# Kernel tuning notes

Measured on AMD Instinct MI355X. Metric: run time of the kernel, lower is better.

## Reference

```python
import jax, jax.numpy as jnp
import numpy as np

EPS = 1e-5
SLOPE = 0.2

def _inorm(x):
    # InstanceNorm2d with affine=False on [B, C, N, 1]: normalize over spatial N per (b, c).
    mu = jnp.mean(x, axis=-1, keepdims=True)
    var = jnp.var(x, axis=-1, keepdims=True)  # biased variance, matches torch InstanceNorm
    return (x - mu) * jax.lax.rsqrt(var + EPS)

def _lrelu(x):
    return jnp.where(x >= 0, x, SLOPE * x)

def _block(W, x):
    # 1x1 conv (channel matmul) -> instance norm -> leaky relu; x: [B, Cin, N]
    return _lrelu(_inorm(jnp.einsum('oc,bcn->bon', W, x)))

def setup_inputs() -> dict:
    key = jax.random.key(0)
    k1, k2, k3, k4, k5 = jax.random.split(key, 5)
    B, C, N = 8, 256, 2048
    feat = jax.random.normal(k1, (B, C, N), dtype=jnp.float32)
    W1 = jax.random.normal(k2, (2 * C, C), dtype=jnp.float32) * (1.0 / np.sqrt(C))
    W2 = jax.random.normal(k3, (2 * C, C), dtype=jnp.float32) * (1.0 / np.sqrt(C))
    W3 = jax.random.normal(k4, (2 * C, C), dtype=jnp.float32) * (1.0 / np.sqrt(C))
    W4 = jax.random.normal(k5, (C, 2 * C), dtype=jnp.float32) * (1.0 / np.sqrt(2 * C))
    return {"feat": feat, "W1": W1, "W2": W2, "W3": W3, "W4": W4}

def reference(feat, W1, W2, W3, W4):
    # feat: [B, C, N]
    x1 = _block(W1, feat)  # [B, 2C, N]
    x2 = _block(W2, feat)  # [B, 2C, N]
    x3 = _block(W3, feat)  # [B, 2C, N]
    # query_key: x1^T @ x2 -> [B, N, N]
    qk = jnp.einsum('bcn,bcm->bnm', x1, x2)
    # x3 @ qk -> [B, 2C, N]; offset attention: subtract from x1
    x4 = x1 - jnp.einsum('bcn,bnm->bcm', x3, qk)
    out = _block(W4, x4)  # [B, C, N]
    return out
```

## Files before the change

### kernel.cpp

```cpp
#include <hip/hip_runtime.h>
#include <stdint.h>


#define LRELU_SLOPE 0.2f
#define EPS_IN 1e-5f

typedef __attribute__((ext_vector_type(8))) short short8v;
typedef __attribute__((ext_vector_type(4))) float f32x4;

__device__ __forceinline__ unsigned short f2bf(float f) {
    unsigned int u = __builtin_bit_cast(unsigned int, f);
    u = (u + 0x7fffu + ((u >> 16) & 1u)) >> 16;
    return (unsigned short)u;
}
__device__ __forceinline__ float bf2f(unsigned short h) {
    return __builtin_bit_cast(float, (unsigned int)h << 16);
}

typedef const __attribute__((address_space(1))) unsigned int* as1_uint_ptr;
typedef __attribute__((address_space(3))) unsigned int* as3_uint_ptr;

#define GLL16(g, l) __builtin_amdgcn_global_load_lds( \
    (as1_uint_ptr)(const void*)(g), (as3_uint_ptr)(void*)(l), 16, 0, 0)

enum { EP_F32 = 0, EP_BF16 = 1, EP_SUB_T_SPLIT = 2, EP_BF16_STATS = 3 };

template<int BM, int BN, int EP>
__global__ __launch_bounds__(256)
void gemm_tn(const unsigned short* __restrict__ A, const unsigned short* __restrict__ B,
             const unsigned short* __restrict__ Dm, void* __restrict__ Cv,
             float2* __restrict__ part,
             int K, int lda, int ldb, int ldd, int ldc,
             int64_t sA, int64_t sB, int64_t sD, int64_t sC)
{
    constexpr int FM = BM / 32, FN = BN / 32;
    const int bz = blockIdx.z;
    A += sA * bz;
    B += sB * bz;

    const int i0 = blockIdx.y * BM;
    const int j0 = blockIdx.x * BN;

    __shared__ __align__(16) unsigned short As[2][BM * 32];
    __shared__ __align__(16) unsigned short Bs[2][BN * 32];

    const int t = threadIdx.x;
    const int w = t >> 6, l = t & 63;
    const int wr = w >> 1, wc = w & 1;
    const int srow = l >> 2, skq = (l & 3) * 8;

    f32x4 acc[FM][FN];
#pragma unroll
    for (int fm = 0; fm < FM; ++fm)
#pragma unroll
        for (int fn = 0; fn < FN; ++fn)
            acc[fm][fn] = (f32x4){0.f, 0.f, 0.f, 0.f};

    const int NT = K / 32;

#pragma unroll
    for (int q = 0; q < BM / 64; ++q) {
        const int seg = w * (BM / 64) + q;
        GLL16(A + (size_t)(i0 + seg * 16 + srow) * lda + skq, &As[0][seg * 512]);
    }
#pragma unroll
    for (int q = 0; q < BN / 64; ++q) {
        const int seg = w * (BN / 64) + q;
        GLL16(B + (size_t)(j0 + seg * 16 + srow) * ldb + skq, &Bs[0][seg * 512]);
    }
    __syncthreads();

    for (int tt = 0; tt < NT; ++tt) {
        const int cur = tt & 1;
        if (tt + 1 < NT) {
            const int k0 = (tt + 1) * 32;
#pragma unroll
            for (int q = 0; q < BM / 64; ++q) {
                const int seg = w * (BM / 64) + q;
                GLL16(A + (size_t)(i0 + seg * 16 + srow) * lda + k0 + skq, &As[cur ^ 1][seg * 512]);
            }
#pragma unroll
            for (int q = 0; q < BN / 64; ++q) {
                const int seg = w * (BN / 64) + q;
                GLL16(B + (size_t)(j0 + seg * 16 + srow) * ldb + k0 + skq, &Bs[cur ^ 1][seg * 512]);
            }
        }
        short8v a[FM], b[FN];
#pragma unroll
        for (int fm = 0; fm < FM; ++fm)
            a[fm] = *(const short8v*)&As[cur][(wr * (BM / 2) + fm * 16 + (l & 15)) * 32 + (l >> 4) * 8];
#pragma unroll
        for (int fn = 0; fn < FN; ++fn)
            b[fn] = *(const short8v*)&Bs[cur][(wc * (BN / 2) + fn * 16 + (l & 15)) * 32 + (l >> 4) * 8];
#pragma unroll
        for (int fm = 0; fm < FM; ++fm)
#pragma unroll
            for (int fn = 0; fn < FN; ++fn)
                acc[fm][fn] = __builtin_amdgcn_mfma_f32_16x16x32_bf16(a[fm], b[fn], acc[fm][fn], 0, 0, 0);
        __syncthreads();
    }

    const int cr4 = (l >> 4) * 4;
    const int cc = l & 15;

    if constexpr (EP == EP_F32) {
        float* C = (float*)Cv + sC * bz;
#pragma unroll
        for (int fm = 0; fm < FM; ++fm)
#pragma unroll
            for (int fn = 0; fn < FN; ++fn)
#pragma unroll
                for (int r = 0; r < 4; ++r)
                    C[(size_t)(i0 + wr * (BM / 2) + fm * 16 + cr4 + r) * ldc +
                      (j0 + wc * (BN / 2) + fn * 16 + cc)] = acc[fm][fn][r];
    } else if constexpr (EP == EP_BF16) {
        unsigned short* C = (unsigned short*)Cv + sC * bz;
#pragma unroll
        for (int fm = 0; fm < FM; ++fm)
#pragma unroll
            for (int fn = 0; fn < FN; ++fn)
#pragma unroll
                for (int r = 0; r < 4; ++r)
                    C[(size_t)(i0 + wr * (BM / 2) + fm * 16 + cr4 + r) * ldc +
                      (j0 + wc * (BN / 2) + fn * 16 + cc)] = f2bf(acc[fm][fn][r]);
    } else if constexpr (EP == EP_SUB_T_SPLIT) {
        const unsigned short* D = Dm + sD * bz;
        unsigned short* C = (unsigned short*)Cv + sC * bz;
#pragma unroll
        for (int fm = 0; fm < FM; ++fm) {
            const int grow0 = i0 + wr * (BM / 2) + fm * 16 + cr4;
#pragma unroll
            for (int fn = 0; fn < FN; ++fn) {
                const int gcol = j0 + wc * (BN / 2) + fn * 16 + cc;
                ushort4 hi4, lo4;
#pragma unroll
                for (int r = 0; r < 4; ++r) {
                    const float sv = bf2f(D[(size_t)(grow0 + r) * ldd + gcol]) - acc[fm][fn][r];
                    const unsigned short h = f2bf(sv);
                    ((unsigned short*)&hi4)[r] = h;
                    ((unsigned short*)&lo4)[r] = f2bf(sv - bf2f(h));
                }
                *(ushort4*)&C[(size_t)gcol * ldc + grow0] = hi4;
                *(ushort4*)&C[(size_t)gcol * ldc + (ldc >> 1) + grow0] = lo4;
            }
        }
    } else {
        unsigned short* C = (unsigned short*)Cv + sC * bz;
        __shared__ float2 wp[2][BM];
#pragma unroll
        for (int fm = 0; fm < FM; ++fm) {
#pragma unroll
            for (int r = 0; r < 4; ++r) {
                float s = 0.f, q = 0.f;
#pragma unroll
                for (int fn = 0; fn < FN; ++fn) {
                    const float v = acc[fm][fn][r];
                    s += v; q += v * v;
                    C[(size_t)(i0 + wr * (BM / 2) + fm * 16 + cr4 + r) * ldc +
                      (j0 + wc * (BN / 2) + fn * 16 + cc)] = f2bf(v);
                }
#pragma unroll
                for (int m = 1; m < 16; m <<= 1) {
                    s += __shfl_xor(s, m, 64);
                    q += __shfl_xor(q, m, 64);
                }
                if ((l & 15) == 0)
                    wp[wc][wr * (BM / 2) + fm * 16 + cr4 + r] = make_float2(s, q);
            }
        }
        __syncthreads();
        if (t < BM) {
            const float2 p0 = wp[0][t], p1 = wp[1][t];
            part[(size_t)(bz * 1536 + i0 + t) * gridDim.x + blockIdx.x] =
                make_float2(p0.x + p1.x, p0.y + p1.y);
        }
    }
}

__global__ __launch_bounds__(256)
void reduce_stats(const float2* __restrict__ part, float2* __restrict__ stats)
{
    const int row = blockIdx.x * 256 + threadIdx.x;
    float S = 0.f, Q = 0.f;
#pragma unroll
    for (int j = 0; j < 16; ++j) {
        const float2 p = part[(size_t)row * 16 + j];
        S += p.x; Q += p.y;
    }
    const float mu = S * (1.0f / 2048.0f);
    const float var = Q * (1.0f / 2048.0f) - mu * mu;
    stats[row] = make_float2(mu, rsqrtf(var + EPS_IN));
}

__device__ __forceinline__ uint4 norm8(uint4 v, float2 st)
{
    const unsigned int wd[4] = {v.x, v.y, v.z, v.w};
    unsigned int o[4];
#pragma unroll
    for (int i = 0; i < 4; ++i) {
        float a = __builtin_bit_cast(float, wd[i] << 16);
        float b = __builtin_bit_cast(float, wd[i] & 0xffff0000u);
        a = (a - st.x) * st.y; a = a >= 0.f ? a : LRELU_SLOPE * a;
        b = (b - st.x) * st.y; b = b >= 0.f ? b : LRELU_SLOPE * b;
        o[i] = (unsigned int)f2bf(a) | ((unsigned int)f2bf(b) << 16);
    }
    return make_uint4(o[0], o[1], o[2], o[3]);
}

__global__ __launch_bounds__(256)
void normx(const unsigned short* __restrict__ ybf, const float2* __restrict__ stats,
           unsigned short* __restrict__ x2T, unsigned short* __restrict__ x1n3)
{
    const int b = blockIdx.x;
    const int t = threadIdx.x;
    if (b < 2048) {
        __shared__ __align__(16) unsigned short tile[64][68];
        const int bx = b & 31, by = (b >> 5) & 7, bz = b >> 8;
        const unsigned short* in = ybf + (size_t)bz * 3145728 + (size_t)512 * 2048;
        unsigned short* outp = x2T + (size_t)bz * 1048576;
        const int r0 = by * 64, c0 = bx * 64;
        const int ir = t >> 4, ic = (t & 15) * 4;
#pragma unroll
        for (int q = 0; q < 4; ++q) {
            const int rr = q * 16 + ir;
            const float2 st = stats[bz * 1536 + 512 + r0 + rr];
            const ushort4 v = *(const ushort4*)&in[(size_t)(r0 + rr) * 2048 + c0 + ic];
            const unsigned short vv[4] = {v.x, v.y, v.z, v.w};
#pragma unroll
            for (int j = 0; j < 4; ++j) {
                float e = (bf2f(vv[j]) - st.x) * st.y;
                e = e >= 0.f ? e : LRELU_SLOPE * e;
                tile[rr][ic + j] = f2bf(e);
            }
        }
        __syncthreads();
        const int n = t & 63, kc = (t >> 6) * 16;
        unsigned short* op = outp + (size_t)(c0 + n) * 512 + r0 + kc;
        unsigned int wo[8];
#pragma unroll
        for (int i = 0; i < 8; ++i)
            wo[i] = (unsigned int)tile[kc + 2 * i][n] | ((unsigned int)tile[kc + 2 * i + 1][n] << 16);
        *(uint4*)op       = make_uint4(wo[0], wo[1], wo[2], wo[3]);
        *(uint4*)(op + 8) = make_uint4(wo[4], wo[5], wo[6], wo[7]);
    } else {
        const int r = b - 2048;
        const int x = r & 1023, bz = r >> 10;
        const int src = (x < 512) ? x : (x + 512);
        const float2 st = stats[bz * 1536 + src];
        const uint4 v = ((const uint4*)(ybf + (size_t)bz * 3145728 + (size_t)src * 2048))[t];
        ((uint4*)(x1n3 + (size_t)bz * 2097152 + (size_t)x * 2048))[t] = norm8(v, st);
    }
}

__global__ __launch_bounds__(256)
void prep(const float* __restrict__ W1, const float* __restrict__ W2,
          const float* __restrict__ W3, const float* __restrict__ W4,
          unsigned short* __restrict__ Wcatb, unsigned short* __restrict__ W4cat,
          const float* __restrict__ feat, unsigned short* __restrict__ featT)
{
    const int b = blockIdx.x;
    const int t = threadIdx.x;
    if (b < 512) {
        const int wsel = b >> 7;
        const int local = ((b & 127) * 256 + t) * 4;
        const float* src = (wsel == 0) ? W1 : (wsel == 1) ? W2 : (wsel == 2) ? W3 : W4;
        const float4 v = *(const float4*)(src + local);
        const ushort4 pk = make_ushort4(f2bf(v.x), f2bf(v.y), f2bf(v.z), f2bf(v.w));
        if (wsel < 3) {
            *(ushort4*)(Wcatb + (size_t)wsel * 131072 + local) = pk;
        } else {
            const int o = local >> 9, c = local & 511;
            *(ushort4*)(W4cat + (size_t)o * 1024 + c)       = pk;
            *(ushort4*)(W4cat + (size_t)o * 1024 + 512 + c) = pk;
        }
    } else {
        __shared__ __align__(16) unsigned short tile[64][68];
        const int r = b - 512;
        const int bx = r & 31, by = (r >> 5) & 3, bz = r >> 7;
        const float* ip0 = feat + (size_t)bz * 524288;
        unsigned short* outp = featT + (size_t)bz * 524288;
        const int r0 = by * 64, c0 = bx * 64;
        const int ir = t >> 4, ic = (t & 15) * 4;
#pragma unroll
        for (int q = 0; q < 4; ++q) {
            const int rr = q * 16 + ir;
            const float4 v = *(const float4*)&ip0[(size_t)(r0 + rr) * 2048 + c0 + ic];
            tile[rr][ic + 0] = f2bf(v.x);
            tile[rr][ic + 1] = f2bf(v.y);
            tile[rr][ic + 2] = f2bf(v.z);
            tile[rr][ic + 3] = f2bf(v.w);
        }
        __syncthreads();
        const int n = t & 63, kc = (t >> 6) * 16;
        unsigned short* op = outp + (size_t)(c0 + n) * 256 + r0 + kc;
        unsigned int wo[8];
#pragma unroll
        for (int i = 0; i < 8; ++i)
            wo[i] = (unsigned int)tile[kc + 2 * i][n] | ((unsigned int)tile[kc + 2 * i + 1][n] << 16);
        *(uint4*)op       = make_uint4(wo[0], wo[1], wo[2], wo[3]);
        *(uint4*)(op + 8) = make_uint4(wo[4], wo[5], wo[6], wo[7]);
    }
}

__global__ __launch_bounds__(256)
void row_norm_lrelu(const float* __restrict__ in, float* __restrict__ out)
{
    const size_t row = blockIdx.x;
    const float4* p = (const float4*)(in + row * 2048);
    float4* q = (float4*)(out + row * 2048);
    const int t = threadIdx.x;

    float4 v0 = p[t];
    float4 v1 = p[t + 256];

    float s  = v0.x + v0.y + v0.z + v0.w + v1.x + v1.y + v1.z + v1.w;
    float ss = v0.x * v0.x + v0.y * v0.y + v0.z * v0.z + v0.w * v0.w +
               v1.x * v1.x + v1.y * v1.y + v1.z * v1.z + v1.w * v1.w;
#pragma unroll
    for (int off = 32; off > 0; off >>= 1) {
        s  += __shfl_down(s, off, 64);
        ss += __shfl_down(ss, off, 64);
    }
    __shared__ float red[10];
    const int wid = t >> 6;
    if ((t & 63) == 0) { red[wid] = s; red[4 + wid] = ss; }
    __syncthreads();
    if (t == 0) {
        const float S  = red[0] + red[1] + red[2] + red[3];
        const float SS = red[4] + red[5] + red[6] + red[7];
        const float mu = S * (1.0f / 2048.0f);
        const float var = SS * (1.0f / 2048.0f) - mu * mu;
        red[8] = mu;
        red[9] = rsqrtf(var + EPS_IN);
    }
    __syncthreads();
    const float mu = red[8], rs = red[9];
#define NRM(x) { float e = ((x) - mu) * rs; (x) = (e >= 0.0f) ? e : LRELU_SLOPE * e; }
    NRM(v0.x) NRM(v0.y) NRM(v0.z) NRM(v0.w)
    NRM(v1.x) NRM(v1.y) NRM(v1.z) NRM(v1.w)
#undef NRM
    q[t] = v0;
    q[t + 256] = v1;
}

extern "C" void kernel_launch(void* const* d_in, const int* in_sizes, int n_in,
                              void* d_out, int out_size, void* d_ws, size_t ws_size,
                              hipStream_t stream)
{
    const float* feat = (const float*)d_in[0];
    const float* W1   = (const float*)d_in[1];
    const float* W2   = (const float*)d_in[2];
    const float* W3   = (const float*)d_in[3];
    const float* W4   = (const float*)d_in[4];
    float* out = (float*)d_out;

    char* w = (char*)d_ws;
    unsigned short* ybf   = (unsigned short*)(w + 0);
    unsigned short* x4Ts  = (unsigned short*)(w + 0);
    float*          z     = (float*)(w + 33554432);
    unsigned short* featT = (unsigned short*)(w + 50331648);
    unsigned short* x2T   = (unsigned short*)(w + 58720256);
    unsigned short* x1n3  = (unsigned short*)(w + 75497472);
    unsigned short* Amb   = (unsigned short*)(w + 109051904);
    unsigned short* Wcatb = (unsigned short*)(w + 113246208);
    unsigned short* W4cat = (unsigned short*)(w + 114032640);
    float2*         part1 = (float2*)(w + 114556928);
    float2*         stats = (float2*)(w + 116129792);

    prep<<<1536, 256, 0, stream>>>(W1, W2, W3, W4, Wcatb, W4cat, feat, featT);

    gemm_tn<128, 128, EP_BF16_STATS><<<dim3(16, 12, 8), 256, 0, stream>>>(
        Wcatb, featT, nullptr, ybf, part1,
        256, 256, 256, 0, 2048, 0, 524288, 0, 3145728);

    reduce_stats<<<48, 256, 0, stream>>>(part1, stats);

    normx<<<10240, 256, 0, stream>>>(ybf, stats, x2T, x1n3);

    gemm_tn<64, 64, EP_BF16><<<dim3(8, 8, 8), 256, 0, stream>>>(
        x1n3 + 1048576 , x1n3 , nullptr, Amb, nullptr,
        2048, 2048, 2048, 0, 512, 2097152, 2097152, 0, 262144);

    gemm_tn<128, 128, EP_SUB_T_SPLIT><<<dim3(16, 4, 8), 256, 0, stream>>>(
        Amb, x2T, x1n3, x4Ts, nullptr,
        512, 512, 512, 2048, 1024, 262144, 1048576, 2097152, 2097152);

    gemm_tn<128, 64, EP_F32><<<dim3(32, 2, 8), 256, 0, stream>>>(
        W4cat, x4Ts, nullptr, z, nullptr,
        1024, 1024, 1024, 0, 2048, 0, 2097152, 0, 524288);

    row_norm_lrelu<<<2048, 256, 0, stream>>>(z, out);
}
```

Measured before the change: 210.4 us.

## Fuse x1/x3 normalization into Gram GEMM and subtract epilogue, drop x1n3 buffer

```diff
diff --git a/kernel.cpp b/kernel.cpp
--- a/kernel.cpp
+++ b/kernel.cpp
@@ -23,13 +23,28 @@
 #define GLL16(g, l) __builtin_amdgcn_global_load_lds( \
     (as1_uint_ptr)(const void*)(g), (as3_uint_ptr)(void*)(l), 16, 0, 0)
 
-enum { EP_F32 = 0, EP_BF16 = 1, EP_SUB_T_SPLIT = 2, EP_BF16_STATS = 3 };
+enum { EP_F32 = 0, EP_BF16_STATS = 1, EP_SUB_T_SPLIT_NORM = 2 };
+
+__device__ __forceinline__ uint4 norm8(uint4 v, float2 st)
+{
+    const unsigned int wd[4] = {v.x, v.y, v.z, v.w};
+    unsigned int o[4];
+#pragma unroll
+    for (int i = 0; i < 4; ++i) {
+        float a = __builtin_bit_cast(float, wd[i] << 16);
+        float b = __builtin_bit_cast(float, wd[i] & 0xffff0000u);
+        a = (a - st.x) * st.y; a = a >= 0.f ? a : LRELU_SLOPE * a;
+        b = (b - st.x) * st.y; b = b >= 0.f ? b : LRELU_SLOPE * b;
+        o[i] = (unsigned int)f2bf(a) | ((unsigned int)f2bf(b) << 16);
+    }
+    return make_uint4(o[0], o[1], o[2], o[3]);
+}
 
 template<int BM, int BN, int EP>
 __global__ __launch_bounds__(256)
 void gemm_tn(const unsigned short* __restrict__ A, const unsigned short* __restrict__ B,
              const unsigned short* __restrict__ Dm, void* __restrict__ Cv,
-             float2* __restrict__ part,
+             const float2* __restrict__ stats, float2* __restrict__ part,
              int K, int lda, int ldb, int ldd, int ldc,
              int64_t sA, int64_t sB, int64_t sD, int64_t sC)
 {
@@ -113,29 +128,24 @@
                 for (int r = 0; r < 4; ++r)
                     C[(size_t)(i0 + wr * (BM / 2) + fm * 16 + cr4 + r) * ldc +
                       (j0 + wc * (BN / 2) + fn * 16 + cc)] = acc[fm][fn][r];
-    } else if constexpr (EP == EP_BF16) {
-        unsigned short* C = (unsigned short*)Cv + sC * bz;
-#pragma unroll
-        for (int fm = 0; fm < FM; ++fm)
-#pragma unroll
-            for (int fn = 0; fn < FN; ++fn)
-#pragma unroll
-                for (int r = 0; r < 4; ++r)
-                    C[(size_t)(i0 + wr * (BM / 2) + fm * 16 + cr4 + r) * ldc +
-                      (j0 + wc * (BN / 2) + fn * 16 + cc)] = f2bf(acc[fm][fn][r]);
-    } else if constexpr (EP == EP_SUB_T_SPLIT) {
+    } else if constexpr (EP == EP_SUB_T_SPLIT_NORM) {
         const unsigned short* D = Dm + sD * bz;
         unsigned short* C = (unsigned short*)Cv + sC * bz;
 #pragma unroll
         for (int fm = 0; fm < FM; ++fm) {
             const int grow0 = i0 + wr * (BM / 2) + fm * 16 + cr4;
+            float2 st[4];
+#pragma unroll
+            for (int r = 0; r < 4; ++r) st[r] = stats[bz * 1536 + grow0 + r];
 #pragma unroll
             for (int fn = 0; fn < FN; ++fn) {
                 const int gcol = j0 + wc * (BN / 2) + fn * 16 + cc;
                 ushort4 hi4, lo4;
 #pragma unroll
                 for (int r = 0; r < 4; ++r) {
-                    const float sv = bf2f(D[(size_t)(grow0 + r) * ldd + gcol]) - acc[fm][fn][r];
+                    float dv = (bf2f(D[(size_t)(grow0 + r) * ldd + gcol]) - st[r].x) * st[r].y;
+                    dv = dv >= 0.f ? dv : LRELU_SLOPE * dv;
+                    const float sv = dv - acc[fm][fn][r];
                     const unsigned short h = f2bf(sv);
                     ((unsigned short*)&hi4)[r] = h;
                     ((unsigned short*)&lo4)[r] = f2bf(sv - bf2f(h));
@@ -178,6 +188,74 @@
 }
 
 __global__ __launch_bounds__(256)
+void gemm_am(const unsigned short* __restrict__ ybf, const float2* __restrict__ stats,
+             unsigned short* __restrict__ Amb)
+{
+    const int bz = blockIdx.z;
+    const unsigned short* Yb = ybf + (size_t)bz * 3145728;
+    const int i0 = blockIdx.y * 64;
+    const int j0 = blockIdx.x * 64;
+
+    __shared__ __align__(16) unsigned short As[64 * 32];
+    __shared__ __align__(16) unsigned short Bs[64 * 32];
+
+    const int t = threadIdx.x, w = t >> 6, l = t & 63;
+    const int wr = w >> 1, wc = w & 1;
+    const int srow = t >> 2;
+    const int skq = (t & 3) * 8;
+
+    const float2 stA = stats[bz * 1536 + 1024 + i0 + srow];
+    const float2 stB = stats[bz * 1536 + j0 + srow];
+    const unsigned short* gA = Yb + (size_t)(1024 + i0 + srow) * 2048 + skq;
+    const unsigned short* gB = Yb + (size_t)(j0 + srow) * 2048 + skq;
+
+    f32x4 acc[2][2];
+#pragma unroll
+    for (int fm = 0; fm < 2; ++fm)
+#pragma unroll
+        for (int fn = 0; fn < 2; ++fn)
+            acc[fm][fn] = (f32x4){0.f, 0.f, 0.f, 0.f};
+
+    uint4 vA = *(const uint4*)gA;
+    uint4 vB = *(const uint4*)gB;
+
+    for (int tt = 0; tt < 64; ++tt) {
+        if (tt) __syncthreads();
+        *(uint4*)&As[srow * 32 + skq] = norm8(vA, stA);
+        *(uint4*)&Bs[srow * 32 + skq] = norm8(vB, stB);
+        if (tt + 1 < 64) {
+            vA = *(const uint4*)(gA + (size_t)(tt + 1) * 32);
+            vB = *(const uint4*)(gB + (size_t)(tt + 1) * 32);
+        }
+        __syncthreads();
+
+        short8v a[2], b[2];
+#pragma unroll
+        for (int fm = 0; fm < 2; ++fm)
+            a[fm] = *(const short8v*)&As[(wr * 32 + fm * 16 + (l & 15)) * 32 + (l >> 4) * 8];
+#pragma unroll
+        for (int fn = 0; fn < 2; ++fn)
+            b[fn] = *(const short8v*)&Bs[(wc * 32 + fn * 16 + (l & 15)) * 32 + (l >> 4) * 8];
+#pragma unroll
+        for (int fm = 0; fm < 2; ++fm)
+#pragma unroll
+            for (int fn = 0; fn < 2; ++fn)
+                acc[fm][fn] = __builtin_amdgcn_mfma_f32_16x16x32_bf16(a[fm], b[fn], acc[fm][fn], 0, 0, 0);
+    }
+
+    unsigned short* C = Amb + (size_t)bz * 262144;
+    const int cr4 = (l >> 4) * 4, cc = l & 15;
+#pragma unroll
+    for (int fm = 0; fm < 2; ++fm)
+#pragma unroll
+        for (int fn = 0; fn < 2; ++fn)
+#pragma unroll
+            for (int r = 0; r < 4; ++r)
+                C[(size_t)(i0 + wr * 32 + fm * 16 + cr4 + r) * 512 +
+                  (j0 + wc * 32 + fn * 16 + cc)] = f2bf(acc[fm][fn][r]);
+}
+
+__global__ __launch_bounds__(256)
 void reduce_stats(const float2* __restrict__ part, float2* __restrict__ stats)
 {
     const int row = blockIdx.x * 256 + threadIdx.x;
@@ -192,64 +270,41 @@
     stats[row] = make_float2(mu, rsqrtf(var + EPS_IN));
 }
 
-__device__ __forceinline__ uint4 norm8(uint4 v, float2 st)
-{
-    const unsigned int wd[4] = {v.x, v.y, v.z, v.w};
-    unsigned int o[4];
-#pragma unroll
-    for (int i = 0; i < 4; ++i) {
-        float a = __builtin_bit_cast(float, wd[i] << 16);
-        float b = __builtin_bit_cast(float, wd[i] & 0xffff0000u);
-        a = (a - st.x) * st.y; a = a >= 0.f ? a : LRELU_SLOPE * a;
-        b = (b - st.x) * st.y; b = b >= 0.f ? b : LRELU_SLOPE * b;
-        o[i] = (unsigned int)f2bf(a) | ((unsigned int)f2bf(b) << 16);
-    }
-    return make_uint4(o[0], o[1], o[2], o[3]);
-}
-
-__global__ __launch_bounds__(256)
-void normx(const unsigned short* __restrict__ ybf, const float2* __restrict__ stats,
-           unsigned short* __restrict__ x2T, unsigned short* __restrict__ x1n3)
-{
-    const int b = blockIdx.x;
-    const int t = threadIdx.x;
-    if (b < 2048) {
-        __shared__ __align__(16) unsigned short tile[64][68];
-        const int bx = b & 31, by = (b >> 5) & 7, bz = b >> 8;
-        const unsigned short* in = ybf + (size_t)bz * 3145728 + (size_t)512 * 2048;
-        unsigned short* outp = x2T + (size_t)bz * 1048576;
-        const int r0 = by * 64, c0 = bx * 64;
-        const int ir = t >> 4, ic = (t & 15) * 4;
-#pragma unroll
-        for (int q = 0; q < 4; ++q) {
-            const int rr = q * 16 + ir;
-            const float2 st = stats[bz * 1536 + 512 + r0 + rr];
-            const ushort4 v = *(const ushort4*)&in[(size_t)(r0 + rr) * 2048 + c0 + ic];
-            const unsigned short vv[4] = {v.x, v.y, v.z, v.w};
-#pragma unroll
-            for (int j = 0; j < 4; ++j) {
-                float e = (bf2f(vv[j]) - st.x) * st.y;
-                e = e >= 0.f ? e : LRELU_SLOPE * e;
-                tile[rr][ic + j] = f2bf(e);
-            }
-        }
-        __syncthreads();
-        const int n = t & 63, kc = (t >> 6) * 16;
-        unsigned short* op = outp + (size_t)(c0 + n) * 512 + r0 + kc;
-        unsigned int wo[8];
-#pragma unroll
-        for (int i = 0; i < 8; ++i)
-            wo[i] = (unsigned int)tile[kc + 2 * i][n] | ((unsigned int)tile[kc + 2 * i + 1][n] << 16);
-        *(uint4*)op       = make_uint4(wo[0], wo[1], wo[2], wo[3]);
-        *(uint4*)(op + 8) = make_uint4(wo[4], wo[5], wo[6], wo[7]);
-    } else {
-        const int r = b - 2048;
-        const int x = r & 1023, bz = r >> 10;
-        const int src = (x < 512) ? x : (x + 512);
-        const float2 st = stats[bz * 1536 + src];
-        const uint4 v = ((const uint4*)(ybf + (size_t)bz * 3145728 + (size_t)src * 2048))[t];
-        ((uint4*)(x1n3 + (size_t)bz * 2097152 + (size_t)x * 2048))[t] = norm8(v, st);
-    }
+__global__ __launch_bounds__(256)
+void transpose_norm_x2(const unsigned short* __restrict__ ybf,
+                       const float2* __restrict__ stats,
+                       unsigned short* __restrict__ x2T)
+{
+    __shared__ __align__(16) unsigned short tile[64][68];
+    const int t = threadIdx.x, bz = blockIdx.z;
+    const unsigned short* in = ybf + (size_t)bz * 3145728 + (size_t)512 * 2048;
+    unsigned short* outp = x2T + (size_t)bz * 1048576;
+    const int r0 = blockIdx.y * 64, c0 = blockIdx.x * 64;
+    const int ir = t >> 4, ic = (t & 15) * 4;
+
+#pragma unroll
+    for (int q = 0; q < 4; ++q) {
+        const int rr = q * 16 + ir;
+        const float2 st = stats[bz * 1536 + 512 + r0 + rr];
+        const ushort4 v = *(const ushort4*)&in[(size_t)(r0 + rr) * 2048 + c0 + ic];
+        const unsigned short vv[4] = {v.x, v.y, v.z, v.w};
+#pragma unroll
+        for (int j = 0; j < 4; ++j) {
+            float e = (bf2f(vv[j]) - st.x) * st.y;
+            e = e >= 0.f ? e : LRELU_SLOPE * e;
+            tile[rr][ic + j] = f2bf(e);
+        }
+    }
+    __syncthreads();
+
+    const int n = t & 63, kc = (t >> 6) * 16;
+    unsigned short* op = outp + (size_t)(c0 + n) * 512 + r0 + kc;
+    unsigned int wo[8];
+#pragma unroll
+    for (int i = 0; i < 8; ++i)
+        wo[i] = (unsigned int)tile[kc + 2 * i][n] | ((unsigned int)tile[kc + 2 * i + 1][n] << 16);
+    *(uint4*)op       = make_uint4(wo[0], wo[1], wo[2], wo[3]);
+    *(uint4*)(op + 8) = make_uint4(wo[4], wo[5], wo[6], wo[7]);
 }
 
 __global__ __launch_bounds__(256)
@@ -356,37 +411,34 @@
 
     char* w = (char*)d_ws;
     unsigned short* ybf   = (unsigned short*)(w + 0);
-    unsigned short* x4Ts  = (unsigned short*)(w + 0);
-    float*          z     = (float*)(w + 33554432);
     unsigned short* featT = (unsigned short*)(w + 50331648);
     unsigned short* x2T   = (unsigned short*)(w + 58720256);
-    unsigned short* x1n3  = (unsigned short*)(w + 75497472);
+    unsigned short* x4Ts  = (unsigned short*)(w + 75497472);
     unsigned short* Amb   = (unsigned short*)(w + 109051904);
     unsigned short* Wcatb = (unsigned short*)(w + 113246208);
     unsigned short* W4cat = (unsigned short*)(w + 114032640);
     float2*         part1 = (float2*)(w + 114556928);
     float2*         stats = (float2*)(w + 116129792);
+    float*          z     = (float*)(w + 116228096);
 
     prep<<<1536, 256, 0, stream>>>(W1, W2, W3, W4, Wcatb, W4cat, feat, featT);
 
     gemm_tn<128, 128, EP_BF16_STATS><<<dim3(16, 12, 8), 256, 0, stream>>>(
-        Wcatb, featT, nullptr, ybf, part1,
+        Wcatb, featT, nullptr, ybf, nullptr, part1,
         256, 256, 256, 0, 2048, 0, 524288, 0, 3145728);
 
     reduce_stats<<<48, 256, 0, stream>>>(part1, stats);
 
-    normx<<<10240, 256, 0, stream>>>(ybf, stats, x2T, x1n3);
-
-    gemm_tn<64, 64, EP_BF16><<<dim3(8, 8, 8), 256, 0, stream>>>(
-        x1n3 + 1048576 , x1n3 , nullptr, Amb, nullptr,
-        2048, 2048, 2048, 0, 512, 2097152, 2097152, 0, 262144);
-
-    gemm_tn<128, 128, EP_SUB_T_SPLIT><<<dim3(16, 4, 8), 256, 0, stream>>>(
-        Amb, x2T, x1n3, x4Ts, nullptr,
-        512, 512, 512, 2048, 1024, 262144, 1048576, 2097152, 2097152);
+    transpose_norm_x2<<<dim3(32, 8, 8), 256, 0, stream>>>(ybf, stats, x2T);
+
+    gemm_am<<<dim3(8, 8, 8), 256, 0, stream>>>(ybf, stats, Amb);
+
+    gemm_tn<128, 128, EP_SUB_T_SPLIT_NORM><<<dim3(16, 4, 8), 256, 0, stream>>>(
+        Amb, x2T, ybf, x4Ts, stats, nullptr,
+        512, 512, 512, 2048, 1024, 262144, 1048576, 3145728, 2097152);
 
     gemm_tn<128, 64, EP_F32><<<dim3(32, 2, 8), 256, 0, stream>>>(
-        W4cat, x4Ts, nullptr, z, nullptr,
+        W4cat, x4Ts, nullptr, z, nullptr, nullptr,
         1024, 1024, 1024, 0, 2048, 0, 2097152, 0, 524288);
 
     row_norm_lrelu<<<2048, 256, 0, stream>>>(z, out);
```

After: 222.6 us. +5.8%, slower.

## Fuse x1 normalization into subtract epilogue and remap grid batch-fastest

Applied to the files above, without the earlier changes.

```diff
diff --git a/kernel.cpp b/kernel.cpp
--- a/kernel.cpp
+++ b/kernel.cpp
@@ -23,23 +23,27 @@
 #define GLL16(g, l) __builtin_amdgcn_global_load_lds( \
     (as1_uint_ptr)(const void*)(g), (as3_uint_ptr)(void*)(l), 16, 0, 0)
 
-enum { EP_F32 = 0, EP_BF16 = 1, EP_SUB_T_SPLIT = 2, EP_BF16_STATS = 3 };
+enum { EP_F32 = 0, EP_BF16 = 1, EP_SUB_T_SPLIT_NORM = 2, EP_BF16_STATS = 3 };
 
 template<int BM, int BN, int EP>
 __global__ __launch_bounds__(256)
 void gemm_tn(const unsigned short* __restrict__ A, const unsigned short* __restrict__ B,
              const unsigned short* __restrict__ Dm, void* __restrict__ Cv,
-             float2* __restrict__ part,
+             const float2* __restrict__ stats, float2* __restrict__ part,
+             int ntx,
              int K, int lda, int ldb, int ldd, int ldc,
              int64_t sA, int64_t sB, int64_t sD, int64_t sC)
 {
     constexpr int FM = BM / 32, FN = BN / 32;
-    const int bz = blockIdx.z;
+    const int bid = blockIdx.x;
+    const int bz = bid & 7;
+    const int rt = bid >> 3;
+    const int tx = rt % ntx, ty = rt / ntx;
     A += sA * bz;
     B += sB * bz;
 
-    const int i0 = blockIdx.y * BM;
-    const int j0 = blockIdx.x * BN;
+    const int i0 = ty * BM;
+    const int j0 = tx * BN;
 
     __shared__ __align__(16) unsigned short As[2][BM * 32];
     __shared__ __align__(16) unsigned short Bs[2][BN * 32];
@@ -123,19 +127,24 @@
                 for (int r = 0; r < 4; ++r)
                     C[(size_t)(i0 + wr * (BM / 2) + fm * 16 + cr4 + r) * ldc +
                       (j0 + wc * (BN / 2) + fn * 16 + cc)] = f2bf(acc[fm][fn][r]);
-    } else if constexpr (EP == EP_SUB_T_SPLIT) {
+    } else if constexpr (EP == EP_SUB_T_SPLIT_NORM) {
         const unsigned short* D = Dm + sD * bz;
         unsigned short* C = (unsigned short*)Cv + sC * bz;
 #pragma unroll
         for (int fm = 0; fm < FM; ++fm) {
             const int grow0 = i0 + wr * (BM / 2) + fm * 16 + cr4;
+            float2 st[4];
+#pragma unroll
+            for (int r = 0; r < 4; ++r) st[r] = stats[bz * 1536 + grow0 + r];
 #pragma unroll
             for (int fn = 0; fn < FN; ++fn) {
                 const int gcol = j0 + wc * (BN / 2) + fn * 16 + cc;
                 ushort4 hi4, lo4;
 #pragma unroll
                 for (int r = 0; r < 4; ++r) {
-                    const float sv = bf2f(D[(size_t)(grow0 + r) * ldd + gcol]) - acc[fm][fn][r];
+                    float dv = (bf2f(D[(size_t)(grow0 + r) * ldd + gcol]) - st[r].x) * st[r].y;
+                    dv = dv >= 0.f ? dv : LRELU_SLOPE * dv;
+                    const float sv = dv - acc[fm][fn][r];
                     const unsigned short h = f2bf(sv);
                     ((unsigned short*)&hi4)[r] = h;
                     ((unsigned short*)&lo4)[r] = f2bf(sv - bf2f(h));
@@ -171,7 +180,7 @@
         __syncthreads();
         if (t < BM) {
             const float2 p0 = wp[0][t], p1 = wp[1][t];
-            part[(size_t)(bz * 1536 + i0 + t) * gridDim.x + blockIdx.x] =
+            part[(size_t)(bz * 1536 + i0 + t) * ntx + tx] =
                 make_float2(p0.x + p1.x, p0.y + p1.y);
         }
     }
@@ -356,11 +365,11 @@
 
     char* w = (char*)d_ws;
     unsigned short* ybf   = (unsigned short*)(w + 0);
-    unsigned short* x4Ts  = (unsigned short*)(w + 0);
-    float*          z     = (float*)(w + 33554432);
+    float*          z     = (float*)(w + 0);
     unsigned short* featT = (unsigned short*)(w + 50331648);
     unsigned short* x2T   = (unsigned short*)(w + 58720256);
     unsigned short* x1n3  = (unsigned short*)(w + 75497472);
+    unsigned short* x4Ts  = (unsigned short*)(w + 75497472);
     unsigned short* Amb   = (unsigned short*)(w + 109051904);
     unsigned short* Wcatb = (unsigned short*)(w + 113246208);
     unsigned short* W4cat = (unsigned short*)(w + 114032640);
@@ -369,24 +378,24 @@
 
     prep<<<1536, 256, 0, stream>>>(W1, W2, W3, W4, Wcatb, W4cat, feat, featT);
 
-    gemm_tn<128, 128, EP_BF16_STATS><<<dim3(16, 12, 8), 256, 0, stream>>>(
-        Wcatb, featT, nullptr, ybf, part1,
+    gemm_tn<128, 128, EP_BF16_STATS><<<1536, 256, 0, stream>>>(
+        Wcatb, featT, nullptr, ybf, nullptr, part1, 16,
         256, 256, 256, 0, 2048, 0, 524288, 0, 3145728);
 
     reduce_stats<<<48, 256, 0, stream>>>(part1, stats);
 
     normx<<<10240, 256, 0, stream>>>(ybf, stats, x2T, x1n3);
 
-    gemm_tn<64, 64, EP_BF16><<<dim3(8, 8, 8), 256, 0, stream>>>(
-        x1n3 + 1048576 , x1n3 , nullptr, Amb, nullptr,
+    gemm_tn<64, 64, EP_BF16><<<512, 256, 0, stream>>>(
+        x1n3 + 1048576 , x1n3 , nullptr, Amb, nullptr, nullptr, 8,
         2048, 2048, 2048, 0, 512, 2097152, 2097152, 0, 262144);
 
-    gemm_tn<128, 128, EP_SUB_T_SPLIT><<<dim3(16, 4, 8), 256, 0, stream>>>(
-        Amb, x2T, x1n3, x4Ts, nullptr,
-        512, 512, 512, 2048, 1024, 262144, 1048576, 2097152, 2097152);
-
-    gemm_tn<128, 64, EP_F32><<<dim3(32, 2, 8), 256, 0, stream>>>(
-        W4cat, x4Ts, nullptr, z, nullptr,
+    gemm_tn<128, 128, EP_SUB_T_SPLIT_NORM><<<512, 256, 0, stream>>>(
+        Amb, x2T, ybf, x4Ts, stats, nullptr, 16,
+        512, 512, 512, 2048, 1024, 262144, 1048576, 3145728, 2097152);
+
+    gemm_tn<128, 64, EP_F32><<<512, 256, 0, stream>>>(
+        W4cat, x4Ts, nullptr, z, nullptr, nullptr, 32,
         1024, 1024, 1024, 0, 2048, 0, 2097152, 0, 524288);
 
     row_norm_lrelu<<<2048, 256, 0, stream>>>(z, out);
```

New measurement: 208.9 us. Within noise of the previous version (-0.7%).
